# Kernel tuning notes

Measured on AMD Instinct MI355X. Metric: run time of the kernel, lower is better.

## Reference

```python
import jax, jax.numpy as jnp
import numpy as np

NUM_OPS = 100_000
NUM_MACH = 512
H = 128
OPF = 6
MF = 2
L = 2
N_PREC = 800_000
N_CHALF = 800_000  # compat edges per direction
EPS = 1e-5


def setup_inputs() -> dict:
    key = jax.random.key(0)
    ks = jax.random.split(key, 20)
    op_features = jax.random.normal(ks[0], (NUM_OPS, OPF), dtype=jnp.float32)
    machine_features = jax.random.normal(ks[1], (NUM_MACH, MF), dtype=jnp.float32)
    prec_src = jax.random.randint(ks[2], (N_PREC,), 0, NUM_OPS, dtype=jnp.int32)
    prec_tgt = jax.random.randint(ks[3], (N_PREC,), 0, NUM_OPS, dtype=jnp.int32)
    precedence_edges = jnp.stack([prec_src, prec_tgt])  # [2, N_PREC]
    op_idx = jax.random.randint(ks[4], (N_CHALF,), 0, NUM_OPS, dtype=jnp.int32)
    m_idx = jax.random.randint(ks[5], (N_CHALF,), 0, NUM_MACH, dtype=jnp.int32)
    # bidirectional pairs in unified node space (machines offset by NUM_OPS)
    src = jnp.concatenate([op_idx, m_idx + NUM_OPS])
    tgt = jnp.concatenate([m_idx + NUM_OPS, op_idx])
    compatibility_edges = jnp.stack([src, tgt])  # [2, 2*N_CHALF]
    s = 0.05
    op_emb_W = jax.random.normal(ks[6], (H, OPF), dtype=jnp.float32) * s
    op_emb_b = jnp.zeros((H,), jnp.float32)
    mach_emb_W = jax.random.normal(ks[7], (H, MF), dtype=jnp.float32) * s
    mach_emb_b = jnp.zeros((H,), jnp.float32)
    prec_W = jax.random.normal(ks[8], (L, H, H), dtype=jnp.float32) * s
    prec_b = jax.random.normal(ks[9], (L, H), dtype=jnp.float32) * s
    compat_W = jax.random.normal(ks[10], (L, H, H), dtype=jnp.float32) * s
    compat_b = jax.random.normal(ks[11], (L, H), dtype=jnp.float32) * s
    op_ln_g = jnp.ones((L, H), jnp.float32)
    op_ln_b = jnp.zeros((L, H), jnp.float32)
    mach_ln_g = jnp.ones((L, H), jnp.float32)
    mach_ln_b = jnp.zeros((L, H), jnp.float32)
    return dict(op_features=op_features, machine_features=machine_features,
                precedence_edges=precedence_edges, compatibility_edges=compatibility_edges,
                op_emb_W=op_emb_W, op_emb_b=op_emb_b, mach_emb_W=mach_emb_W, mach_emb_b=mach_emb_b,
                prec_W=prec_W, prec_b=prec_b, compat_W=compat_W, compat_b=compat_b,
                op_ln_g=op_ln_g, op_ln_b=op_ln_b, mach_ln_g=mach_ln_g, mach_ln_b=mach_ln_b)


def _layer_norm(x, g, b):
    mu = jnp.mean(x, axis=-1, keepdims=True)
    var = jnp.mean(jnp.square(x - mu), axis=-1, keepdims=True)
    return (x - mu) * jax.lax.rsqrt(var + EPS) * g + b


def _scatter_mean(vals, idx, mask, n):
    # vals [E,H], idx [E], mask [E] bool (or None); mean over incoming edges, count clamped >= 1
    if mask is not None:
        vals = jnp.where(mask[:, None], vals, 0.0)
        idx = jnp.where(mask, idx, 0)
        ones = mask.astype(vals.dtype)
    else:
        ones = jnp.ones(idx.shape, vals.dtype)
    sums = jax.ops.segment_sum(vals, idx, num_segments=n)
    cnts = jax.ops.segment_sum(ones, idx, num_segments=n)
    return sums / jnp.maximum(cnts, 1.0)[:, None]


def _forward(op_features, machine_features, precedence_edges, compatibility_edges,
             op_emb_W, op_emb_b, mach_emb_W, mach_emb_b,
             prec_W, prec_b, compat_W, compat_b,
             op_ln_g, op_ln_b, mach_ln_g, mach_ln_b):
    num_ops = op_features.shape[0]
    num_mach = machine_features.shape[0]
    op_emb = op_features @ op_emb_W.T + op_emb_b
    mach_emb = machine_features @ mach_emb_W.T + mach_emb_b

    p_src, p_tgt = precedence_edges[0], precedence_edges[1]
    c_src, c_tgt = compatibility_edges[0], compatibility_edges[1]
    op2m = (c_src < num_ops) & (c_tgt >= num_ops)
    m2o = (c_src >= num_ops) & (c_tgt < num_ops)
    o2m_src = jnp.where(op2m, c_src, 0)
    o2m_tgt = jnp.where(op2m, c_tgt - num_ops, 0)
    m2o_src = jnp.where(m2o, c_src - num_ops, 0)
    m2o_tgt = jnp.where(m2o, c_tgt, 0)

    for l in range(L):
        # precedence (op -> op): linear-then-gather == gather-then-linear
        op_t = op_emb @ prec_W[l].T + prec_b[l]            # [num_ops, H]
        op_emb_prec = _scatter_mean(op_t[p_src], p_tgt, None, num_ops)
        # compatibility, shared linear for both directions
        op_c = op_emb @ compat_W[l].T + compat_b[l]        # [num_ops, H]
        mach_c = mach_emb @ compat_W[l].T + compat_b[l]    # [num_mach, H]
        mach_emb_compat = _scatter_mean(op_c[o2m_src], o2m_tgt, op2m, num_mach)
        op_emb_compat = _scatter_mean(mach_c[m2o_src], m2o_tgt, m2o, num_ops)
        op_emb = _layer_norm(op_emb + op_emb_prec + op_emb_compat, op_ln_g[l], op_ln_b[l])
        mach_emb = _layer_norm(mach_emb + mach_emb_compat, mach_ln_g[l], mach_ln_b[l])
    return op_emb, mach_emb


def reference(op_features, machine_features, precedence_edges, compatibility_edges,
              op_emb_W, op_emb_b, mach_emb_W, mach_emb_b,
              prec_W, prec_b, compat_W, compat_b,
              op_ln_g, op_ln_b, mach_ln_g, mach_ln_b):
    return _forward(op_features, machine_features, precedence_edges, compatibility_edges,
                    op_emb_W, op_emb_b, mach_emb_W, mach_emb_b,
                    prec_W, prec_b, compat_W, compat_b,
                    op_ln_g, op_ln_b, mach_ln_g, mach_ln_b)
```

## Files before the change

kernel.cpp:

```cpp
#include <hip/hip_runtime.h>
#include <hip/hip_bf16.h>

#define NUM_OPS   100000
#define NUM_MACH  512
#define HDIM      128
#define P1        100352
#define NHIST     200704
#define NBLK      196
#define NCOARSE   784
#define NBC       256
#define NBM       256
#define MHWORDS   (NUM_MACH * NBM)
#define NBLK_M    128

typedef short short8 __attribute__((ext_vector_type(8)));
typedef float floatx4 __attribute__((ext_vector_type(4)));

__device__ __forceinline__ unsigned short f2bf(float f) {
    unsigned u = __float_as_uint(f);
    unsigned r = (u + 0x7FFFu + ((u >> 16) & 1u)) >> 16;
    return (unsigned short)r;
}
__device__ __forceinline__ float bf2f(unsigned short u) {
    return __uint_as_float(((unsigned)u) << 16);
}

__global__ void k_embed(const float* __restrict__ F,
                        const float* __restrict__ W,
                        const float* __restrict__ b,
                        float* __restrict__ out,
                        unsigned short* __restrict__ outb, int M, int FD) {
    int idx = blockIdx.x * blockDim.x + threadIdx.x;
    if (idx >= M * HDIM) return;
    int r = idx >> 7, h = idx & 127;
    const float* f = F + (size_t)r * FD;
    const float* w = W + (size_t)h * FD;
    float s = b[h];
    for (int i = 0; i < FD; ++i) s += f[i] * w[i];
    out[idx] = s;
    if (outb) outb[idx] = f2bf(s);
}

__global__ void k_wconv(const float* __restrict__ Wp, const float* __restrict__ Wc,
                        unsigned short* __restrict__ Wb) {
    int i = blockIdx.x * blockDim.x + threadIdx.x;
    if (i >= 2 * 128 * 256) return;
    int l = i >> 15, h = (i >> 8) & 127, k = i & 255;
    float v = (k < 128) ? Wp[(size_t)l * 16384 + h * 128 + k]
                        : Wc[(size_t)l * 16384 + h * 128 + (k - 128)];
    Wb[i] = f2bf(v);
}

__global__ __launch_bounds__(256) void k_chist(const int* __restrict__ prec_e, int nprec,
                                               const int* __restrict__ comp_e, int E,
                                               int* __restrict__ blockhist) {
    __shared__ int h[NCOARSE];
    for (int i = threadIdx.x; i < NCOARSE; i += 256) h[i] = 0;
    __syncthreads();
    int NT = nprec + E;
    int ch = (NT + NBC - 1) / NBC;
    int i0 = blockIdx.x * ch, i1 = min(NT, i0 + ch);
    for (int i = i0 + threadIdx.x; i < i1; i += 256) {
        int key = (i < nprec) ? prec_e[nprec + i] : (P1 + comp_e[i - nprec]);
        atomicAdd(&h[key >> 8], 1);
    }
    __syncthreads();
    for (int i = threadIdx.x; i < NCOARSE; i += 256)
        blockhist[i * NBC + blockIdx.x] = h[i];
}

__global__ __launch_bounds__(256) void k_cfill(const int* __restrict__ prec_e, int nprec,
                                               const int* __restrict__ comp_e, int E, int M,
                                               const int* __restrict__ scan,
                                               int* __restrict__ pairs) {
    __shared__ int cur[NCOARSE];
    for (int i = threadIdx.x; i < NCOARSE; i += 256) cur[i] = scan[i * NBC + blockIdx.x];
    __syncthreads();
    int NT = nprec + E;
    int ch = (NT + NBC - 1) / NBC;
    int i0 = blockIdx.x * ch, i1 = min(NT, i0 + ch);
    for (int i = i0 + threadIdx.x; i < i1; i += 256) {
        int key, val;
        if (i < nprec) { key = prec_e[nprec + i]; val = prec_e[i]; }
        else { int e = i - nprec; key = P1 + comp_e[e]; val = comp_e[E + e] - M; }
        int pos = atomicAdd(&cur[key >> 8], 1);
        pairs[pos] = (val << 8) | (key & 255);
    }
}

__global__ __launch_bounds__(256) void k_fine(const int* __restrict__ scan,
                                              const int* __restrict__ pairs, int NT,
                                              int* __restrict__ rs,
                                              int* __restrict__ bucket_all) {
    __shared__ int hh[256];
    __shared__ int ex[256];
    __shared__ int cu[256];
    int b = blockIdx.x, t = threadIdx.x;
    int s = scan[b * NBC];
    int e = (b == NCOARSE - 1) ? NT : scan[(b + 1) * NBC];
    hh[t] = 0;
    __syncthreads();
    for (int i = s + t; i < e; i += 256) atomicAdd(&hh[pairs[i] & 255], 1);
    __syncthreads();
    int v = hh[t];
    ex[t] = v; __syncthreads();
    for (int o = 1; o < 256; o <<= 1) {
        int x = (t >= o) ? ex[t - o] : 0; __syncthreads();
        ex[t] += x; __syncthreads();
    }
    int start = s + ex[t] - v;
    rs[b * 256 + t] = start;
    cu[t] = start;
    __syncthreads();
    for (int i = s + t; i < e; i += 256) {
        int p = pairs[i];
        int pos = atomicAdd(&cu[p & 255], 1);
        bucket_all[pos] = ((unsigned)p) >> 8;
    }
}

__global__ __launch_bounds__(256) void k_mhist(const int* __restrict__ comp_e, int E, int M,
                                               int* __restrict__ blockhist) {
    __shared__ int h[NUM_MACH];
    for (int i = threadIdx.x; i < NUM_MACH; i += 256) h[i] = 0;
    __syncthreads();
    int blk = blockIdx.x;
    int ch = (E + NBM - 1) / NBM;
    int e0 = blk * ch, e1 = min(E, e0 + ch);
    for (int e = e0 + threadIdx.x; e < e1; e += 256)
        atomicAdd(&h[comp_e[E + e] - M], 1);
    __syncthreads();
    for (int i = threadIdx.x; i < NUM_MACH; i += 256)
        blockhist[i * NBM + blk] = h[i];
}

__global__ __launch_bounds__(256) void k_blocksum(const int* __restrict__ arr, int* __restrict__ partial) {
    __shared__ int sh[256];
    int b = blockIdx.x, t = threadIdx.x;
    int4 v = *(const int4*)(arr + b * 1024 + t * 4);
    sh[t] = v.x + v.y + v.z + v.w;
    __syncthreads();
    for (int o = 128; o; o >>= 1) { if (t < o) sh[t] += sh[t + o]; __syncthreads(); }
    if (!t) partial[b] = sh[0];
}

__global__ __launch_bounds__(256) void k_scanpart(const int* __restrict__ partial, int n,
                                                  int* __restrict__ block_off) {
    __shared__ int sh[256];
    int t = threadIdx.x;
    int v = (t < n) ? partial[t] : 0;
    sh[t] = v; __syncthreads();
    for (int o = 1; o < 256; o <<= 1) {
        int x = (t >= o) ? sh[t - o] : 0; __syncthreads();
        sh[t] += x; __syncthreads();
    }
    if (t < n) block_off[t] = sh[t] - v;
}

__global__ __launch_bounds__(256) void k_scanwrite(const int* __restrict__ arr,
                                                   const int* __restrict__ block_off,
                                                   int* __restrict__ rs, int* __restrict__ cur) {
    __shared__ int sh[256];
    int b = blockIdx.x, t = threadIdx.x;
    int base_i = b * 1024 + t * 4;
    int4 v = *(const int4*)(arr + base_i);
    int tsum = v.x + v.y + v.z + v.w;
    sh[t] = tsum; __syncthreads();
    for (int o = 1; o < 256; o <<= 1) {
        int x = (t >= o) ? sh[t - o] : 0; __syncthreads();
        sh[t] += x; __syncthreads();
    }
    int off = block_off[b] + sh[t] - tsum;
    int4 r; r.x = off; r.y = off + v.x; r.z = off + v.x + v.y; r.w = off + v.x + v.y + v.z;
    *(int4*)(rs + base_i) = r;
    if (cur) *(int4*)(cur + base_i) = r;
}

__global__ void k_machrs(const int* __restrict__ moff, int* __restrict__ mach_rs, int E) {
    int t = threadIdx.x;
    for (int m = t; m < NUM_MACH; m += 256) mach_rs[m] = moff[m * NBM];
    if (t == 0) mach_rs[NUM_MACH] = E;
}

__global__ __launch_bounds__(256) void k_fill_mach(const int* __restrict__ comp_e, int E, int M,
                                                   const int* __restrict__ moff,
                                                   int* __restrict__ bucket_mach) {
    __shared__ int cur[NUM_MACH];
    int blk = blockIdx.x;
    for (int i = threadIdx.x; i < NUM_MACH; i += 256) cur[i] = moff[i * NBM + blk];
    __syncthreads();
    int ch = (E + NBM - 1) / NBM;
    int e0 = blk * ch, e1 = min(E, e0 + ch);
    for (int e = e0 + threadIdx.x; e < e1; e += 256) {
        int m = comp_e[E + e] - M;
        int op = comp_e[e];
        int pos = atomicAdd(&cur[m], 1);
        bucket_mach[pos] = op;
    }
}

__global__ __launch_bounds__(256) void k_agg_op(
    const unsigned short* __restrict__ op_ebf, const float* __restrict__ mach_emb,
    const int* __restrict__ rs, const int* __restrict__ bucket_all,
    unsigned short* __restrict__ Ab, int* __restrict__ flags, int M) {
    int wave = threadIdx.x >> 6, lane = threadIdx.x & 63;
    int r = blockIdx.x * 4 + wave;
    if (r >= M) return;
    int h = lane * 2;

    float a0 = 0.f, a1 = 0.f;
    int s0 = rs[r], e0 = rs[r + 1];
    for (int base = s0; base < e0; base += 64) {
        int cnt = min(64, e0 - base);
        int idx = (lane < cnt) ? bucket_all[base + lane] : 0;
        for (int j = 0; j < cnt; j += 4) {
            int i0 = __shfl(idx, j);
            int i1 = __shfl(idx, j + 1);
            int i2 = __shfl(idx, j + 2);
            int i3 = __shfl(idx, j + 3);
            ushort2 v0 = *(const ushort2*)(op_ebf + (size_t)i0 * HDIM + h);
            ushort2 v1 = *(const ushort2*)(op_ebf + (size_t)i1 * HDIM + h);
            ushort2 v2 = *(const ushort2*)(op_ebf + (size_t)i2 * HDIM + h);
            ushort2 v3 = *(const ushort2*)(op_ebf + (size_t)i3 * HDIM + h);
            a0 += bf2f(v0.x); a1 += bf2f(v0.y);
            if (j + 1 < cnt) { a0 += bf2f(v1.x); a1 += bf2f(v1.y); }
            if (j + 2 < cnt) { a0 += bf2f(v2.x); a1 += bf2f(v2.y); }
            if (j + 3 < cnt) { a0 += bf2f(v3.x); a1 += bf2f(v3.y); }
        }
    }
    float pinv = 1.f / fmaxf((float)(e0 - s0), 1.f);

    float b0 = 0.f, b1 = 0.f;
    int s1 = rs[P1 + r], e1 = rs[P1 + r + 1];
    for (int base = s1; base < e1; base += 64) {
        int cnt = min(64, e1 - base);
        int idx = (lane < cnt) ? bucket_all[base + lane] : 0;
        for (int j = 0; j < cnt; j += 4) {
            int i0 = __shfl(idx, j);
            int i1 = __shfl(idx, j + 1);
            int i2 = __shfl(idx, j + 2);
            int i3 = __shfl(idx, j + 3);
            float2 v0 = *(const float2*)(mach_emb + (size_t)i0 * HDIM + h);
            float2 v1 = *(const float2*)(mach_emb + (size_t)i1 * HDIM + h);
            float2 v2 = *(const float2*)(mach_emb + (size_t)i2 * HDIM + h);
            float2 v3 = *(const float2*)(mach_emb + (size_t)i3 * HDIM + h);
            b0 += v0.x; b1 += v0.y;
            if (j + 1 < cnt) { b0 += v1.x; b1 += v1.y; }
            if (j + 2 < cnt) { b0 += v2.x; b1 += v2.y; }
            if (j + 3 < cnt) { b0 += v3.x; b1 += v3.y; }
        }
    }
    float cinv = 1.f / fmaxf((float)(e1 - s1), 1.f);

    ushort2 pa, pb;
    pa.x = f2bf(a0 * pinv); pa.y = f2bf(a1 * pinv);
    pb.x = f2bf(b0 * cinv); pb.y = f2bf(b1 * cinv);
    *(ushort2*)(Ab + (size_t)r * 256 + h)       = pa;
    *(ushort2*)(Ab + (size_t)r * 256 + 128 + h) = pb;
    if (lane == 0) flags[r] = (e0 > s0 ? 1 : 0) | (e1 > s1 ? 2 : 0);
}

__global__ __launch_bounds__(256) void k_gemm_mfma(
    const unsigned short* __restrict__ Ab, const float* __restrict__ emb,
    const unsigned short* __restrict__ Wb,
    const float* __restrict__ bp, const float* __restrict__ bc,
    const int* __restrict__ flags,
    const float* __restrict__ g, const float* __restrict__ bt,
    float* __restrict__ dst, unsigned short* __restrict__ dstb, int M) {
    int wave = threadIdx.x >> 6, lane = threadIdx.x & 63;
    int m0 = blockIdx.x * 64 + wave * 16;
    if (m0 >= M) return;
    int quad = lane >> 4, col = lane & 15;

    floatx4 acc[8];
#pragma unroll
    for (int t = 0; t < 8; ++t) acc[t] = (floatx4){0.f, 0.f, 0.f, 0.f};

    const short* Arow  = (const short*)(Ab + (size_t)(m0 + col) * 256);
    const short* Wbase = (const short*)Wb;

#pragma unroll
    for (int ks = 0; ks < 8; ++ks) {
        short8 a = *(const short8*)(Arow + ks * 32 + quad * 8);
#pragma unroll
        for (int t = 0; t < 8; ++t) {
            short8 b = *(const short8*)(Wbase + (size_t)(t * 16 + col) * 256 + ks * 32 + quad * 8);
            acc[t] = __builtin_amdgcn_mfma_f32_16x16x32_bf16(a, b, acc[t], 0, 0, 0);
        }
    }

    float bpv[8], bcv[8], gv[8], btv[8];
#pragma unroll
    for (int t = 0; t < 8; ++t) {
        int c = t * 16 + col;
        bpv[t] = bp[c]; bcv[t] = bc[c]; gv[t] = g[c]; btv[t] = bt[c];
    }
#pragma unroll
    for (int reg = 0; reg < 4; ++reg) {
        int r = m0 + quad * 4 + reg;
        int fl = flags[r];
        float fp = (fl & 1) ? 1.f : 0.f, fc = (fl & 2) ? 1.f : 0.f;
        float x[8]; float s = 0.f, q = 0.f;
#pragma unroll
        for (int t = 0; t < 8; ++t) {
            float v = acc[t][reg] + emb[(size_t)r * HDIM + t * 16 + col] + fp * bpv[t] + fc * bcv[t];
            x[t] = v; s += v; q += v * v;
        }
#pragma unroll
        for (int msk = 1; msk < 16; msk <<= 1) { s += __shfl_xor(s, msk); q += __shfl_xor(q, msk); }
        float mu = s * (1.f / 128.f);
        float rstd = rsqrtf(fmaxf(q * (1.f / 128.f) - mu * mu, 0.f) + 1e-5f);
#pragma unroll
        for (int t = 0; t < 8; ++t) {
            float y = (x[t] - mu) * rstd * gv[t] + btv[t];
            dst[(size_t)r * HDIM + t * 16 + col] = y;
            if (dstb) dstb[(size_t)r * HDIM + t * 16 + col] = f2bf(y);
        }
    }
}

__global__ __launch_bounds__(256) void k_mach_gather(
    const int* __restrict__ mach_rs, const int* __restrict__ bucket_mach,
    const unsigned short* __restrict__ op_ebf, float* __restrict__ mach_sum) {
    int m = blockIdx.x;
    int t = threadIdx.x;
    int wave = t >> 6, lane = t & 63;
    int h = lane * 2;
    int s0 = mach_rs[m], e0 = mach_rs[m + 1];
    float a0 = 0.f, a1 = 0.f;
    for (int base = s0 + (blockIdx.y * 4 + wave) * 64; base < e0; base += gridDim.y * 256) {
        int cnt = min(64, e0 - base);
        int idx = (lane < cnt) ? bucket_mach[base + lane] : 0;
        for (int j = 0; j < cnt; j += 4) {
            int i0 = __shfl(idx, j);
            int i1 = __shfl(idx, j + 1);
            int i2 = __shfl(idx, j + 2);
            int i3 = __shfl(idx, j + 3);
            ushort2 v0 = *(const ushort2*)(op_ebf + (size_t)i0 * HDIM + h);
            ushort2 v1 = *(const ushort2*)(op_ebf + (size_t)i1 * HDIM + h);
            ushort2 v2 = *(const ushort2*)(op_ebf + (size_t)i2 * HDIM + h);
            ushort2 v3 = *(const ushort2*)(op_ebf + (size_t)i3 * HDIM + h);
            a0 += bf2f(v0.x); a1 += bf2f(v0.y);
            if (j + 1 < cnt) { a0 += bf2f(v1.x); a1 += bf2f(v1.y); }
            if (j + 2 < cnt) { a0 += bf2f(v2.x); a1 += bf2f(v2.y); }
            if (j + 3 < cnt) { a0 += bf2f(v3.x); a1 += bf2f(v3.y); }
        }
    }
    atomicAdd(&mach_sum[m * HDIM + h], a0);
    atomicAdd(&mach_sum[m * HDIM + h + 1], a1);
}

__global__ __launch_bounds__(128) void k_mach_update(
    const float* __restrict__ mach_emb, const float* __restrict__ mach_sum,
    const int* __restrict__ mach_rs,
    const float* __restrict__ Wc, const float* __restrict__ bc,
    const float* __restrict__ g, const float* __restrict__ bt,
    float* __restrict__ dst) {
    __shared__ float row[HDIM];
    __shared__ float red[4];
    int m = blockIdx.x, t = threadIdx.x;
    int cnt = mach_rs[m + 1] - mach_rs[m];
    float sc = (cnt > 0) ? 1.f / (float)cnt : 0.f;
    row[t] = mach_sum[m * HDIM + t] * sc;
    __syncthreads();
    float dot = bc[t];
    const float* w = Wc + (size_t)t * HDIM;
#pragma unroll 8
    for (int k = 0; k < HDIM; ++k) dot += row[k] * w[k];
    float x = mach_emb[m * HDIM + t] + ((cnt > 0) ? dot : 0.f);
    float s = x, q = x * x;
#pragma unroll
    for (int o = 32; o; o >>= 1) { s += __shfl_xor(s, o); q += __shfl_xor(q, o); }
    int wv = t >> 6;
    if ((t & 63) == 0) { red[wv * 2] = s; red[wv * 2 + 1] = q; }
    __syncthreads();
    s = red[0] + red[2]; q = red[1] + red[3];
    float mu = s * (1.f / 128.f);
    float rstd = rsqrtf(fmaxf(q * (1.f / 128.f) - mu * mu, 0.f) + 1e-5f);
    dst[m * HDIM + t] = (x - mu) * rstd * g[t] + bt[t];
}

extern "C" void kernel_launch(void* const* d_in, const int* in_sizes, int n_in,
                              void* d_out, int out_size, void* d_ws, size_t ws_size,
                              hipStream_t stream) {
    const float* op_feat    = (const float*)d_in[0];
    const float* m_feat     = (const float*)d_in[1];
    const int*   prec_e     = (const int*)d_in[2];
    const int*   comp_e     = (const int*)d_in[3];
    const float* op_emb_W   = (const float*)d_in[4];
    const float* op_emb_b   = (const float*)d_in[5];
    const float* mach_emb_W = (const float*)d_in[6];
    const float* mach_emb_b = (const float*)d_in[7];
    const float* prec_W     = (const float*)d_in[8];
    const float* prec_b     = (const float*)d_in[9];
    const float* compat_W   = (const float*)d_in[10];
    const float* compat_b   = (const float*)d_in[11];
    const float* op_ln_g    = (const float*)d_in[12];
    const float* op_ln_b    = (const float*)d_in[13];
    const float* mach_ln_g  = (const float*)d_in[14];
    const float* mach_ln_b  = (const float*)d_in[15];
    float* out = (float*)d_out;

    const int M = NUM_OPS, NM = NUM_MACH;
    const int nprec = in_sizes[2] / 2;
    const int ncomp = in_sizes[3] / 2;
    const int E = ncomp / 2;
    const int NT = nprec + E;

    float* ws = (float*)d_ws;
    size_t o = 0;
    float* op_emb   = ws + o; o += (size_t)M * HDIM;
    unsigned short* op_ebf = (unsigned short*)(ws + o); o += (size_t)M * 64;
    unsigned short* Ab = (unsigned short*)(ws + o); o += (size_t)M * 128;
    unsigned short* Wb = (unsigned short*)(ws + o); o += 32768;
    float* mach_emb = ws + o; o += (size_t)NM * HDIM;
    float* mach_sum = ws + o; o += (size_t)NM * HDIM;
    int* ip = (int*)(ws + o);
    size_t io = 0;
    int* chist     = ip + io; io += NHIST;
    int* rs        = ip + io; io += NHIST;
    int* cscan     = ip + io; io += NHIST;
    int* blockhist = ip + io; io += MHWORDS;
    int* moff      = ip + io; io += MHWORDS;
    int* mach_rs   = ip + io; io += NM + 8;
    int* partialA  = ip + io; io += 256;
    int* block_offA= ip + io; io += 256;
    int* partialB  = ip + io; io += 256;
    int* block_offB= ip + io; io += 256;
    int* flags     = ip + io; io += M;
    int* pairs     = ip + io; io += (size_t)NT;
    int* bucket_all  = ip + io; io += (size_t)NT;
    int* bucket_mach = ip + io; io += (size_t)E;

    k_chist<<<NBC, 256, 0, stream>>>(prec_e, nprec, comp_e, E, chist);
    k_mhist<<<NBM, 256, 0, stream>>>(comp_e, E, M, blockhist);
    k_blocksum<<<NBLK, 256, 0, stream>>>(chist, partialA);
    k_scanpart<<<1, 256, 0, stream>>>(partialA, NBLK, block_offA);
    k_scanwrite<<<NBLK, 256, 0, stream>>>(chist, block_offA, cscan, nullptr);
    k_blocksum<<<NBLK_M, 256, 0, stream>>>(blockhist, partialB);
    k_scanpart<<<1, 256, 0, stream>>>(partialB, NBLK_M, block_offB);
    k_scanwrite<<<NBLK_M, 256, 0, stream>>>(blockhist, block_offB, moff, nullptr);
    k_machrs<<<1, 256, 0, stream>>>(moff, mach_rs, E);
    k_cfill<<<NBC, 256, 0, stream>>>(prec_e, nprec, comp_e, E, M, cscan, pairs);
    k_fine<<<NCOARSE, 256, 0, stream>>>(cscan, pairs, NT, rs, bucket_all);
    k_fill_mach<<<NBM, 256, 0, stream>>>(comp_e, E, M, moff, bucket_mach);

    k_embed<<<(M * HDIM + 255) / 256, 256, 0, stream>>>(op_feat, op_emb_W, op_emb_b, op_emb, op_ebf, M, 6);
    k_embed<<<(NM * HDIM + 255) / 256, 256, 0, stream>>>(m_feat, mach_emb_W, mach_emb_b, mach_emb, nullptr, NM, 2);
    k_wconv<<<(2 * 128 * 256 + 255) / 256, 256, 0, stream>>>(prec_W, compat_W, Wb);

    for (int l = 0; l < 2; ++l) {
        int last = (l == 1);
        const float* bpl = prec_b   + (size_t)l * HDIM;
        const float* Wc  = compat_W + (size_t)l * HDIM * HDIM;
        const float* bcl = compat_b + (size_t)l * HDIM;

        hipMemsetAsync(mach_sum, 0, (size_t)NM * HDIM * sizeof(float), stream);

        k_agg_op<<<(M + 3) / 4, 256, 0, stream>>>(op_ebf, mach_emb, rs, bucket_all, Ab, flags, M);
        k_mach_gather<<<dim3(NM, 4), 256, 0, stream>>>(mach_rs, bucket_mach, op_ebf, mach_sum);

        k_gemm_mfma<<<(M + 63) / 64, 256, 0, stream>>>(
            Ab, op_emb, Wb + (size_t)l * 128 * 256, bpl, bcl, flags,
            op_ln_g + (size_t)l * HDIM, op_ln_b + (size_t)l * HDIM,
            last ? out : op_emb, last ? nullptr : op_ebf, M);

        k_mach_update<<<NM, 128, 0, stream>>>(
            mach_emb, mach_sum, mach_rs, Wc, bcl,
            mach_ln_g + (size_t)l * HDIM, mach_ln_b + (size_t)l * HDIM,
            last ? (out + (size_t)M * HDIM) : mach_emb);
    }
}
```

Before: 583.2 us.

## Fuse op aggregation into MFMA GEMM kernel via swizzled LDS tile

The per-op neighbour aggregation (precedence and compatibility means) moves into the GEMM+LayerNorm kernel. Each wave gathers its 16 rows into a swizzled 64x256 bf16 shared-memory tile, and edge-presence flags are packed into a register. This removes the global Ab intermediate and flags buffer round trip and one launch per layer. The bf16 op embedding is now ping-ponged between two buffers, because the fused kernel writes new embeddings while other rows still read the old ones, and the machine gather is reordered to run afterwards. The cost is that each wave gathers its 16 rows one after another, and the 32KB of LDS per block lowers occupancy, which may reduce memory-level parallelism for the random gathers.

Result: slower. 732.6 us (+25.6%).

```diff
diff --git a/kernel.cpp b/kernel.cpp
--- a/kernel.cpp
+++ b/kernel.cpp
@@ -199,89 +199,90 @@
     }
 }
 
-__global__ __launch_bounds__(256) void k_agg_op(
+__global__ __launch_bounds__(256) void k_fused(
     const unsigned short* __restrict__ op_ebf, const float* __restrict__ mach_emb,
     const int* __restrict__ rs, const int* __restrict__ bucket_all,
-    unsigned short* __restrict__ Ab, int* __restrict__ flags, int M) {
-    int wave = threadIdx.x >> 6, lane = threadIdx.x & 63;
-    int r = blockIdx.x * 4 + wave;
-    if (r >= M) return;
-    int h = lane * 2;
-
-    float a0 = 0.f, a1 = 0.f;
-    int s0 = rs[r], e0 = rs[r + 1];
-    for (int base = s0; base < e0; base += 64) {
-        int cnt = min(64, e0 - base);
-        int idx = (lane < cnt) ? bucket_all[base + lane] : 0;
-        for (int j = 0; j < cnt; j += 4) {
-            int i0 = __shfl(idx, j);
-            int i1 = __shfl(idx, j + 1);
-            int i2 = __shfl(idx, j + 2);
-            int i3 = __shfl(idx, j + 3);
-            ushort2 v0 = *(const ushort2*)(op_ebf + (size_t)i0 * HDIM + h);
-            ushort2 v1 = *(const ushort2*)(op_ebf + (size_t)i1 * HDIM + h);
-            ushort2 v2 = *(const ushort2*)(op_ebf + (size_t)i2 * HDIM + h);
-            ushort2 v3 = *(const ushort2*)(op_ebf + (size_t)i3 * HDIM + h);
-            a0 += bf2f(v0.x); a1 += bf2f(v0.y);
-            if (j + 1 < cnt) { a0 += bf2f(v1.x); a1 += bf2f(v1.y); }
-            if (j + 2 < cnt) { a0 += bf2f(v2.x); a1 += bf2f(v2.y); }
-            if (j + 3 < cnt) { a0 += bf2f(v3.x); a1 += bf2f(v3.y); }
-        }
-    }
-    float pinv = 1.f / fmaxf((float)(e0 - s0), 1.f);
-
-    float b0 = 0.f, b1 = 0.f;
-    int s1 = rs[P1 + r], e1 = rs[P1 + r + 1];
-    for (int base = s1; base < e1; base += 64) {
-        int cnt = min(64, e1 - base);
-        int idx = (lane < cnt) ? bucket_all[base + lane] : 0;
-        for (int j = 0; j < cnt; j += 4) {
-            int i0 = __shfl(idx, j);
-            int i1 = __shfl(idx, j + 1);
-            int i2 = __shfl(idx, j + 2);
-            int i3 = __shfl(idx, j + 3);
-            float2 v0 = *(const float2*)(mach_emb + (size_t)i0 * HDIM + h);
-            float2 v1 = *(const float2*)(mach_emb + (size_t)i1 * HDIM + h);
-            float2 v2 = *(const float2*)(mach_emb + (size_t)i2 * HDIM + h);
-            float2 v3 = *(const float2*)(mach_emb + (size_t)i3 * HDIM + h);
-            b0 += v0.x; b1 += v0.y;
-            if (j + 1 < cnt) { b0 += v1.x; b1 += v1.y; }
-            if (j + 2 < cnt) { b0 += v2.x; b1 += v2.y; }
-            if (j + 3 < cnt) { b0 += v3.x; b1 += v3.y; }
-        }
-    }
-    float cinv = 1.f / fmaxf((float)(e1 - s1), 1.f);
-
-    ushort2 pa, pb;
-    pa.x = f2bf(a0 * pinv); pa.y = f2bf(a1 * pinv);
-    pb.x = f2bf(b0 * cinv); pb.y = f2bf(b1 * cinv);
-    *(ushort2*)(Ab + (size_t)r * 256 + h)       = pa;
-    *(ushort2*)(Ab + (size_t)r * 256 + 128 + h) = pb;
-    if (lane == 0) flags[r] = (e0 > s0 ? 1 : 0) | (e1 > s1 ? 2 : 0);
-}
-
-__global__ __launch_bounds__(256) void k_gemm_mfma(
-    const unsigned short* __restrict__ Ab, const float* __restrict__ emb,
+    const float* __restrict__ emb,
     const unsigned short* __restrict__ Wb,
     const float* __restrict__ bp, const float* __restrict__ bc,
-    const int* __restrict__ flags,
     const float* __restrict__ g, const float* __restrict__ bt,
     float* __restrict__ dst, unsigned short* __restrict__ dstb, int M) {
+    __shared__ unsigned short At[64 * 256];
     int wave = threadIdx.x >> 6, lane = threadIdx.x & 63;
     int m0 = blockIdx.x * 64 + wave * 16;
     if (m0 >= M) return;
+    int h = lane * 2;
+    unsigned fl_packed = 0;
+
+    for (int i = 0; i < 16; ++i) {
+        int r = m0 + i;
+        int ri = wave * 16 + i;
+
+        float a0 = 0.f, a1 = 0.f;
+        int s0 = rs[r], e0 = rs[r + 1];
+        for (int base = s0; base < e0; base += 64) {
+            int cnt = min(64, e0 - base);
+            int idx = (lane < cnt) ? bucket_all[base + lane] : 0;
+            for (int j = 0; j < cnt; j += 4) {
+                int i0 = __shfl(idx, j);
+                int i1 = __shfl(idx, j + 1);
+                int i2 = __shfl(idx, j + 2);
+                int i3 = __shfl(idx, j + 3);
+                ushort2 v0 = *(const ushort2*)(op_ebf + (size_t)i0 * HDIM + h);
+                ushort2 v1 = *(const ushort2*)(op_ebf + (size_t)i1 * HDIM + h);
+                ushort2 v2 = *(const ushort2*)(op_ebf + (size_t)i2 * HDIM + h);
+                ushort2 v3 = *(const ushort2*)(op_ebf + (size_t)i3 * HDIM + h);
+                a0 += bf2f(v0.x); a1 += bf2f(v0.y);
+                if (j + 1 < cnt) { a0 += bf2f(v1.x); a1 += bf2f(v1.y); }
+                if (j + 2 < cnt) { a0 += bf2f(v2.x); a1 += bf2f(v2.y); }
+                if (j + 3 < cnt) { a0 += bf2f(v3.x); a1 += bf2f(v3.y); }
+            }
+        }
+        float pinv = 1.f / fmaxf((float)(e0 - s0), 1.f);
+
+        float b0 = 0.f, b1 = 0.f;
+        int s1 = rs[P1 + r], e1 = rs[P1 + r + 1];
+        for (int base = s1; base < e1; base += 64) {
+            int cnt = min(64, e1 - base);
+            int idx = (lane < cnt) ? bucket_all[base + lane] : 0;
+            for (int j = 0; j < cnt; j += 4) {
+                int i0 = __shfl(idx, j);
+                int i1 = __shfl(idx, j + 1);
+                int i2 = __shfl(idx, j + 2);
+                int i3 = __shfl(idx, j + 3);
+                float2 v0 = *(const float2*)(mach_emb + (size_t)i0 * HDIM + h);
+                float2 v1 = *(const float2*)(mach_emb + (size_t)i1 * HDIM + h);
+                float2 v2 = *(const float2*)(mach_emb + (size_t)i2 * HDIM + h);
+                float2 v3 = *(const float2*)(mach_emb + (size_t)i3 * HDIM + h);
+                b0 += v0.x; b1 += v0.y;
+                if (j + 1 < cnt) { b0 += v1.x; b1 += v1.y; }
+                if (j + 2 < cnt) { b0 += v2.x; b1 += v2.y; }
+                if (j + 3 < cnt) { b0 += v3.x; b1 += v3.y; }
+            }
+        }
+        float cinv = 1.f / fmaxf((float)(e1 - s1), 1.f);
+
+        ushort2 pa, pb;
+        pa.x = f2bf(a0 * pinv); pa.y = f2bf(a1 * pinv);
+        pb.x = f2bf(b0 * cinv); pb.y = f2bf(b1 * cinv);
+        unsigned sw = (ri & 7) << 4;
+        *(ushort2*)((char*)At + ri * 512 + ((lane * 4) ^ sw))       = pa;
+        *(ushort2*)((char*)At + ri * 512 + ((256 + lane * 4) ^ sw)) = pb;
+        fl_packed |= ((e0 > s0 ? 1u : 0u) | (e1 > s1 ? 2u : 0u)) << (2 * i);
+    }
+
     int quad = lane >> 4, col = lane & 15;
+    int ri = wave * 16 + col;
+    unsigned swr = (ri & 7) << 4;
 
     floatx4 acc[8];
 #pragma unroll
     for (int t = 0; t < 8; ++t) acc[t] = (floatx4){0.f, 0.f, 0.f, 0.f};
 
-    const short* Arow  = (const short*)(Ab + (size_t)(m0 + col) * 256);
     const short* Wbase = (const short*)Wb;
-
 #pragma unroll
     for (int ks = 0; ks < 8; ++ks) {
-        short8 a = *(const short8*)(Arow + ks * 32 + quad * 8);
+        short8 a = *(const short8*)((const char*)At + ri * 512 + ((ks * 64 + quad * 16) ^ swr));
 #pragma unroll
         for (int t = 0; t < 8; ++t) {
             short8 b = *(const short8*)(Wbase + (size_t)(t * 16 + col) * 256 + ks * 32 + quad * 8);
@@ -298,7 +299,7 @@
 #pragma unroll
     for (int reg = 0; reg < 4; ++reg) {
         int r = m0 + quad * 4 + reg;
-        int fl = flags[r];
+        int fl = (fl_packed >> ((quad * 4 + reg) * 2)) & 3;
         float fp = (fl & 1) ? 1.f : 0.f, fc = (fl & 2) ? 1.f : 0.f;
         float x[8]; float s = 0.f, q = 0.f;
 #pragma unroll
@@ -410,8 +411,8 @@
     float* ws = (float*)d_ws;
     size_t o = 0;
     float* op_emb   = ws + o; o += (size_t)M * HDIM;
-    unsigned short* op_ebf = (unsigned short*)(ws + o); o += (size_t)M * 64;
-    unsigned short* Ab = (unsigned short*)(ws + o); o += (size_t)M * 128;
+    unsigned short* op_ebfA = (unsigned short*)(ws + o); o += (size_t)M * 64;
+    unsigned short* op_ebfB = (unsigned short*)(ws + o); o += (size_t)M * 64;
     unsigned short* Wb = (unsigned short*)(ws + o); o += 32768;
     float* mach_emb = ws + o; o += (size_t)NM * HDIM;
     float* mach_sum = ws + o; o += (size_t)NM * HDIM;
@@ -427,7 +428,6 @@
     int* block_offA= ip + io; io += 256;
     int* partialB  = ip + io; io += 256;
     int* block_offB= ip + io; io += 256;
-    int* flags     = ip + io; io += M;
     int* pairs     = ip + io; io += (size_t)NT;
     int* bucket_all  = ip + io; io += (size_t)NT;
     int* bucket_mach = ip + io; io += (size_t)E;
@@ -445,25 +445,27 @@
     k_fine<<<NCOARSE, 256, 0, stream>>>(cscan, pairs, NT, rs, bucket_all);
     k_fill_mach<<<NBM, 256, 0, stream>>>(comp_e, E, M, moff, bucket_mach);
 
-    k_embed<<<(M * HDIM + 255) / 256, 256, 0, stream>>>(op_feat, op_emb_W, op_emb_b, op_emb, op_ebf, M, 6);
+    k_embed<<<(M * HDIM + 255) / 256, 256, 0, stream>>>(op_feat, op_emb_W, op_emb_b, op_emb, op_ebfA, M, 6);
     k_embed<<<(NM * HDIM + 255) / 256, 256, 0, stream>>>(m_feat, mach_emb_W, mach_emb_b, mach_emb, nullptr, NM, 2);
     k_wconv<<<(2 * 128 * 256 + 255) / 256, 256, 0, stream>>>(prec_W, compat_W, Wb);
 
     for (int l = 0; l < 2; ++l) {
         int last = (l == 1);
+        const unsigned short* ebf_src = (l == 0) ? op_ebfA : op_ebfB;
+        unsigned short* ebf_dst = (l == 0) ? op_ebfB : nullptr;
         const float* bpl = prec_b   + (size_t)l * HDIM;
         const float* Wc  = compat_W + (size_t)l * HDIM * HDIM;
         const float* bcl = compat_b + (size_t)l * HDIM;
 
         hipMemsetAsync(mach_sum, 0, (size_t)NM * HDIM * sizeof(float), stream);
 
-        k_agg_op<<<(M + 3) / 4, 256, 0, stream>>>(op_ebf, mach_emb, rs, bucket_all, Ab, flags, M);
-        k_mach_gather<<<dim3(NM, 4), 256, 0, stream>>>(mach_rs, bucket_mach, op_ebf, mach_sum);
-
-        k_gemm_mfma<<<(M + 63) / 64, 256, 0, stream>>>(
-            Ab, op_emb, Wb + (size_t)l * 128 * 256, bpl, bcl, flags,
+        k_fused<<<(M + 63) / 64, 256, 0, stream>>>(
+            ebf_src, mach_emb, rs, bucket_all, op_emb,
+            Wb + (size_t)l * 128 * 256, bpl, bcl,
             op_ln_g + (size_t)l * HDIM, op_ln_b + (size_t)l * HDIM,
-            last ? out : op_emb, last ? nullptr : op_ebf, M);
+            last ? out : op_emb, ebf_dst, M);
+
+        k_mach_gather<<<dim3(NM, 4), 256, 0, stream>>>(mach_rs, bucket_mach, ebf_src, mach_sum);
 
         k_mach_update<<<NM, 128, 0, stream>>>(
             mach_emb, mach_sum, mach_rs, Wc, bcl,
```

## Merge preprocessing and aggregation kernels to cut launch count

Applied to the files above, without the earlier changes.

Several small kernels are fused into fewer launches. The coarse and machine histograms are built in one pass, and both scans are batched into single blocksum/scanpart/scanwrite launches. The fine bucket fill is merged with the machine fill, the three embedding and weight-conversion kernels become one, and op aggregation is merged with the machine gather, which now uses 16-byte short8 loads. The aim is to remove launch overhead and serialization between small kernels, at the cost of branchy mixed-role grids and a machine partition tied to the NT chunking.

Result: no change. 579.1 us (-0.7%).

```diff
diff --git a/kernel.cpp b/kernel.cpp
--- a/kernel.cpp
+++ b/kernel.cpp
@@ -12,6 +12,7 @@
 #define NBM       256
 #define MHWORDS   (NUM_MACH * NBM)
 #define NBLK_M    128
+#define NBLK_T    (NBLK + NBLK_M)
 
 typedef short short8 __attribute__((ext_vector_type(8)));
 typedef float floatx4 __attribute__((ext_vector_type(4)));
@@ -25,48 +26,68 @@
     return __uint_as_float(((unsigned)u) << 16);
 }
 
-__global__ void k_embed(const float* __restrict__ F,
-                        const float* __restrict__ W,
-                        const float* __restrict__ b,
-                        float* __restrict__ out,
-                        unsigned short* __restrict__ outb, int M, int FD) {
+__global__ void k_prep(const float* __restrict__ Fo, const float* __restrict__ Fm,
+                       const float* __restrict__ Wo, const float* __restrict__ bo,
+                       const float* __restrict__ Wm, const float* __restrict__ bm,
+                       const float* __restrict__ Wp, const float* __restrict__ Wc,
+                       float* __restrict__ op_emb, unsigned short* __restrict__ op_ebf,
+                       float* __restrict__ mach_emb, unsigned short* __restrict__ Wb) {
     int idx = blockIdx.x * blockDim.x + threadIdx.x;
-    if (idx >= M * HDIM) return;
-    int r = idx >> 7, h = idx & 127;
-    const float* f = F + (size_t)r * FD;
-    const float* w = W + (size_t)h * FD;
-    float s = b[h];
-    for (int i = 0; i < FD; ++i) s += f[i] * w[i];
-    out[idx] = s;
-    if (outb) outb[idx] = f2bf(s);
-}
-
-__global__ void k_wconv(const float* __restrict__ Wp, const float* __restrict__ Wc,
-                        unsigned short* __restrict__ Wb) {
-    int i = blockIdx.x * blockDim.x + threadIdx.x;
-    if (i >= 2 * 128 * 256) return;
-    int l = i >> 15, h = (i >> 8) & 127, k = i & 255;
-    float v = (k < 128) ? Wp[(size_t)l * 16384 + h * 128 + k]
-                        : Wc[(size_t)l * 16384 + h * 128 + (k - 128)];
-    Wb[i] = f2bf(v);
-}
-
-__global__ __launch_bounds__(256) void k_chist(const int* __restrict__ prec_e, int nprec,
-                                               const int* __restrict__ comp_e, int E,
-                                               int* __restrict__ blockhist) {
-    __shared__ int h[NCOARSE];
-    for (int i = threadIdx.x; i < NCOARSE; i += 256) h[i] = 0;
+    if (idx < NUM_OPS * HDIM) {
+        int r = idx >> 7, h = idx & 127;
+        const float* f = Fo + (size_t)r * 6;
+        const float* w = Wo + (size_t)h * 6;
+        float s = bo[h];
+#pragma unroll
+        for (int i = 0; i < 6; ++i) s += f[i] * w[i];
+        op_emb[idx] = s;
+        op_ebf[idx] = f2bf(s);
+        return;
+    }
+    idx -= NUM_OPS * HDIM;
+    if (idx < NUM_MACH * HDIM) {
+        int r = idx >> 7, h = idx & 127;
+        const float* f = Fm + (size_t)r * 2;
+        const float* w = Wm + (size_t)h * 2;
+        mach_emb[idx] = bm[h] + f[0] * w[0] + f[1] * w[1];
+        return;
+    }
+    idx -= NUM_MACH * HDIM;
+    if (idx < 2 * 128 * 256) {
+        int l = idx >> 15, h = (idx >> 8) & 127, k = idx & 255;
+        float v = (k < 128) ? Wp[(size_t)l * 16384 + h * 128 + k]
+                            : Wc[(size_t)l * 16384 + h * 128 + (k - 128)];
+        Wb[idx] = f2bf(v);
+    }
+}
+
+__global__ __launch_bounds__(256) void k_front(const int* __restrict__ prec_e, int nprec,
+                                               const int* __restrict__ comp_e, int E, int M,
+                                               int* __restrict__ chist_bh,
+                                               int* __restrict__ mach_bh) {
+    __shared__ int hc[NCOARSE];
+    __shared__ int hm[NUM_MACH];
+    for (int i = threadIdx.x; i < NCOARSE; i += 256) hc[i] = 0;
+    for (int i = threadIdx.x; i < NUM_MACH; i += 256) hm[i] = 0;
     __syncthreads();
     int NT = nprec + E;
     int ch = (NT + NBC - 1) / NBC;
     int i0 = blockIdx.x * ch, i1 = min(NT, i0 + ch);
     for (int i = i0 + threadIdx.x; i < i1; i += 256) {
-        int key = (i < nprec) ? prec_e[nprec + i] : (P1 + comp_e[i - nprec]);
-        atomicAdd(&h[key >> 8], 1);
+        int key;
+        if (i < nprec) key = prec_e[nprec + i];
+        else {
+            int e = i - nprec;
+            key = P1 + comp_e[e];
+            atomicAdd(&hm[comp_e[E + e] - M], 1);
+        }
+        atomicAdd(&hc[key >> 8], 1);
     }
     __syncthreads();
     for (int i = threadIdx.x; i < NCOARSE; i += 256)
-        blockhist[i * NBC + blockIdx.x] = h[i];
+        chist_bh[i * NBC + blockIdx.x] = hc[i];
+    for (int i = threadIdx.x; i < NUM_MACH; i += 256)
+        mach_bh[i * NBC + blockIdx.x] = hm[i];
 }
 
 __global__ __launch_bounds__(256) void k_cfill(const int* __restrict__ prec_e, int nprec,
@@ -88,52 +109,6 @@
     }
 }
 
-__global__ __launch_bounds__(256) void k_fine(const int* __restrict__ scan,
-                                              const int* __restrict__ pairs, int NT,
-                                              int* __restrict__ rs,
-                                              int* __restrict__ bucket_all) {
-    __shared__ int hh[256];
-    __shared__ int ex[256];
-    __shared__ int cu[256];
-    int b = blockIdx.x, t = threadIdx.x;
-    int s = scan[b * NBC];
-    int e = (b == NCOARSE - 1) ? NT : scan[(b + 1) * NBC];
-    hh[t] = 0;
-    __syncthreads();
-    for (int i = s + t; i < e; i += 256) atomicAdd(&hh[pairs[i] & 255], 1);
-    __syncthreads();
-    int v = hh[t];
-    ex[t] = v; __syncthreads();
-    for (int o = 1; o < 256; o <<= 1) {
-        int x = (t >= o) ? ex[t - o] : 0; __syncthreads();
-        ex[t] += x; __syncthreads();
-    }
-    int start = s + ex[t] - v;
-    rs[b * 256 + t] = start;
-    cu[t] = start;
-    __syncthreads();
-    for (int i = s + t; i < e; i += 256) {
-        int p = pairs[i];
-        int pos = atomicAdd(&cu[p & 255], 1);
-        bucket_all[pos] = ((unsigned)p) >> 8;
-    }
-}
-
-__global__ __launch_bounds__(256) void k_mhist(const int* __restrict__ comp_e, int E, int M,
-                                               int* __restrict__ blockhist) {
-    __shared__ int h[NUM_MACH];
-    for (int i = threadIdx.x; i < NUM_MACH; i += 256) h[i] = 0;
-    __syncthreads();
-    int blk = blockIdx.x;
-    int ch = (E + NBM - 1) / NBM;
-    int e0 = blk * ch, e1 = min(E, e0 + ch);
-    for (int e = e0 + threadIdx.x; e < e1; e += 256)
-        atomicAdd(&h[comp_e[E + e] - M], 1);
-    __syncthreads();
-    for (int i = threadIdx.x; i < NUM_MACH; i += 256)
-        blockhist[i * NBM + blk] = h[i];
-}
-
 __global__ __launch_bounds__(256) void k_blocksum(const int* __restrict__ arr, int* __restrict__ partial) {
     __shared__ int sh[256];
     int b = blockIdx.x, t = threadIdx.x;
@@ -144,22 +119,24 @@
     if (!t) partial[b] = sh[0];
 }
 
-__global__ __launch_bounds__(256) void k_scanpart(const int* __restrict__ partial, int n,
+__global__ __launch_bounds__(256) void k_scanpart(const int* __restrict__ partial,
                                                   int* __restrict__ block_off) {
     __shared__ int sh[256];
     int t = threadIdx.x;
-    int v = (t < n) ? partial[t] : 0;
+    int seg0 = blockIdx.x ? NBLK : 0;
+    int n    = blockIdx.x ? NBLK_M : NBLK;
+    int v = (t < n) ? partial[seg0 + t] : 0;
     sh[t] = v; __syncthreads();
     for (int o = 1; o < 256; o <<= 1) {
         int x = (t >= o) ? sh[t - o] : 0; __syncthreads();
         sh[t] += x; __syncthreads();
     }
-    if (t < n) block_off[t] = sh[t] - v;
+    if (t < n) block_off[seg0 + t] = sh[t] - v;
 }
 
 __global__ __launch_bounds__(256) void k_scanwrite(const int* __restrict__ arr,
                                                    const int* __restrict__ block_off,
-                                                   int* __restrict__ rs, int* __restrict__ cur) {
+                                                   int* __restrict__ rs) {
     __shared__ int sh[256];
     int b = blockIdx.x, t = threadIdx.x;
     int base_i = b * 1024 + t * 4;
@@ -173,91 +150,164 @@
     int off = block_off[b] + sh[t] - tsum;
     int4 r; r.x = off; r.y = off + v.x; r.z = off + v.x + v.y; r.w = off + v.x + v.y + v.z;
     *(int4*)(rs + base_i) = r;
-    if (cur) *(int4*)(cur + base_i) = r;
-}
-
-__global__ void k_machrs(const int* __restrict__ moff, int* __restrict__ mach_rs, int E) {
+}
+
+__global__ __launch_bounds__(256) void k_finefill(const int* __restrict__ scans, int NT,
+                                                  const int* __restrict__ pairs,
+                                                  int* __restrict__ rs,
+                                                  int* __restrict__ bucket_all,
+                                                  const int* __restrict__ comp_e, int E, int M,
+                                                  int* __restrict__ bucket_mach,
+                                                  int* __restrict__ mach_rs) {
     int t = threadIdx.x;
-    for (int m = t; m < NUM_MACH; m += 256) mach_rs[m] = moff[m * NBM];
-    if (t == 0) mach_rs[NUM_MACH] = E;
-}
-
-__global__ __launch_bounds__(256) void k_fill_mach(const int* __restrict__ comp_e, int E, int M,
-                                                   const int* __restrict__ moff,
-                                                   int* __restrict__ bucket_mach) {
-    __shared__ int cur[NUM_MACH];
-    int blk = blockIdx.x;
-    for (int i = threadIdx.x; i < NUM_MACH; i += 256) cur[i] = moff[i * NBM + blk];
-    __syncthreads();
-    int ch = (E + NBM - 1) / NBM;
-    int e0 = blk * ch, e1 = min(E, e0 + ch);
-    for (int e = e0 + threadIdx.x; e < e1; e += 256) {
-        int m = comp_e[E + e] - M;
-        int op = comp_e[e];
-        int pos = atomicAdd(&cur[m], 1);
-        bucket_mach[pos] = op;
-    }
-}
-
-__global__ __launch_bounds__(256) void k_agg_op(
+    if (blockIdx.x < NCOARSE) {
+        __shared__ int hh[256];
+        __shared__ int ex[256];
+        __shared__ int cu[256];
+        int b = blockIdx.x;
+        int s = scans[b * NBC];
+        int e = (b == NCOARSE - 1) ? NT : scans[(b + 1) * NBC];
+        hh[t] = 0;
+        __syncthreads();
+        for (int i = s + t; i < e; i += 256) atomicAdd(&hh[pairs[i] & 255], 1);
+        __syncthreads();
+        int v = hh[t];
+        ex[t] = v; __syncthreads();
+        for (int o = 1; o < 256; o <<= 1) {
+            int x = (t >= o) ? ex[t - o] : 0; __syncthreads();
+            ex[t] += x; __syncthreads();
+        }
+        int start = s + ex[t] - v;
+        rs[b * 256 + t] = start;
+        cu[t] = start;
+        __syncthreads();
+        for (int i = s + t; i < e; i += 256) {
+            int p = pairs[i];
+            int pos = atomicAdd(&cu[p & 255], 1);
+            bucket_all[pos] = ((unsigned)p) >> 8;
+        }
+    } else {
+        __shared__ int cur[NUM_MACH];
+        int blk = blockIdx.x - NCOARSE;
+        const int* moff = scans + NHIST;
+        for (int i = t; i < NUM_MACH; i += 256) cur[i] = moff[i * NBM + blk];
+        if (blk == 0) {
+            for (int m = t; m < NUM_MACH; m += 256) mach_rs[m] = moff[m * NBM];
+            if (t == 0) mach_rs[NUM_MACH] = E;
+        }
+        __syncthreads();
+        int nprec = NT - E;
+        int chNT = (NT + NBC - 1) / NBC;
+        int e0 = blk * chNT - nprec;       if (e0 < 0) e0 = 0;
+        int e1 = (blk + 1) * chNT - nprec; if (e1 > E) e1 = E;
+        for (int e = e0 + t; e < e1; e += 256) {
+            int m = comp_e[E + e] - M;
+            int op = comp_e[e];
+            int pos = atomicAdd(&cur[m], 1);
+            bucket_mach[pos] = op;
+        }
+    }
+}
+
+__global__ __launch_bounds__(256) void k_aggmg(
     const unsigned short* __restrict__ op_ebf, const float* __restrict__ mach_emb,
     const int* __restrict__ rs, const int* __restrict__ bucket_all,
-    unsigned short* __restrict__ Ab, int* __restrict__ flags, int M) {
+    unsigned short* __restrict__ Ab, int* __restrict__ flags, int M,
+    const int* __restrict__ mach_rs, const int* __restrict__ bucket_mach,
+    float* __restrict__ mach_sum, int nb_agg) {
     int wave = threadIdx.x >> 6, lane = threadIdx.x & 63;
-    int r = blockIdx.x * 4 + wave;
-    if (r >= M) return;
-    int h = lane * 2;
-
-    float a0 = 0.f, a1 = 0.f;
-    int s0 = rs[r], e0 = rs[r + 1];
-    for (int base = s0; base < e0; base += 64) {
+
+    if ((int)blockIdx.x < nb_agg) {
+        int r = blockIdx.x * 4 + wave;
+        if (r >= M) return;
+        int h = lane * 2;
+
+        float a0 = 0.f, a1 = 0.f;
+        int s0 = rs[r], e0 = rs[r + 1];
+        for (int base = s0; base < e0; base += 64) {
+            int cnt = min(64, e0 - base);
+            int idx = (lane < cnt) ? bucket_all[base + lane] : 0;
+            for (int j = 0; j < cnt; j += 4) {
+                int i0 = __shfl(idx, j);
+                int i1 = __shfl(idx, j + 1);
+                int i2 = __shfl(idx, j + 2);
+                int i3 = __shfl(idx, j + 3);
+                ushort2 v0 = *(const ushort2*)(op_ebf + (size_t)i0 * HDIM + h);
+                ushort2 v1 = *(const ushort2*)(op_ebf + (size_t)i1 * HDIM + h);
+                ushort2 v2 = *(const ushort2*)(op_ebf + (size_t)i2 * HDIM + h);
+                ushort2 v3 = *(const ushort2*)(op_ebf + (size_t)i3 * HDIM + h);
+                a0 += bf2f(v0.x); a1 += bf2f(v0.y);
+                if (j + 1 < cnt) { a0 += bf2f(v1.x); a1 += bf2f(v1.y); }
+                if (j + 2 < cnt) { a0 += bf2f(v2.x); a1 += bf2f(v2.y); }
+                if (j + 3 < cnt) { a0 += bf2f(v3.x); a1 += bf2f(v3.y); }
+            }
+        }
+        float pinv = 1.f / fmaxf((float)(e0 - s0), 1.f);
+
+        float b0 = 0.f, b1 = 0.f;
+        int s1 = rs[P1 + r], e1 = rs[P1 + r + 1];
+        for (int base = s1; base < e1; base += 64) {
+            int cnt = min(64, e1 - base);
+            int idx = (lane < cnt) ? bucket_all[base + lane] : 0;
+            for (int j = 0; j < cnt; j += 4) {
+                int i0 = __shfl(idx, j);
+                int i1 = __shfl(idx, j + 1);
+                int i2 = __shfl(idx, j + 2);
+                int i3 = __shfl(idx, j + 3);
+                float2 v0 = *(const float2*)(mach_emb + (size_t)i0 * HDIM + h);
+                float2 v1 = *(const float2*)(mach_emb + (size_t)i1 * HDIM + h);
+                float2 v2 = *(const float2*)(mach_emb + (size_t)i2 * HDIM + h);
+                float2 v3 = *(const float2*)(mach_emb + (size_t)i3 * HDIM + h);
+                b0 += v0.x; b1 += v0.y;
+                if (j + 1 < cnt) { b0 += v1.x; b1 += v1.y; }
+                if (j + 2 < cnt) { b0 += v2.x; b1 += v2.y; }
+                if (j + 3 < cnt) { b0 += v3.x; b1 += v3.y; }
+            }
+        }
+        float cinv = 1.f / fmaxf((float)(e1 - s1), 1.f);
+
+        ushort2 pa, pb;
+        pa.x = f2bf(a0 * pinv); pa.y = f2bf(a1 * pinv);
+        pb.x = f2bf(b0 * cinv); pb.y = f2bf(b1 * cinv);
+        *(ushort2*)(Ab + (size_t)r * 256 + h)       = pa;
+        *(ushort2*)(Ab + (size_t)r * 256 + 128 + h) = pb;
+        if (lane == 0) flags[r] = (e0 > s0 ? 1 : 0) | (e1 > s1 ? 2 : 0);
+        return;
+    }
+
+    int b2 = blockIdx.x - nb_agg;
+    int m  = b2 & 511;
+    int yq = b2 >> 9;
+    int g  = lane >> 4;
+    int d  = (lane & 15) * 8;
+    int s0 = mach_rs[m], e0 = mach_rs[m + 1];
+    float a[8];
+#pragma unroll
+    for (int k = 0; k < 8; ++k) a[k] = 0.f;
+
+    for (int base = s0 + (yq * 4 + wave) * 64; base < e0; base += 1024) {
         int cnt = min(64, e0 - base);
-        int idx = (lane < cnt) ? bucket_all[base + lane] : 0;
+        int idx = (lane < cnt) ? bucket_mach[base + lane] : 0;
         for (int j = 0; j < cnt; j += 4) {
-            int i0 = __shfl(idx, j);
-            int i1 = __shfl(idx, j + 1);
-            int i2 = __shfl(idx, j + 2);
-            int i3 = __shfl(idx, j + 3);
-            ushort2 v0 = *(const ushort2*)(op_ebf + (size_t)i0 * HDIM + h);
-            ushort2 v1 = *(const ushort2*)(op_ebf + (size_t)i1 * HDIM + h);
-            ushort2 v2 = *(const ushort2*)(op_ebf + (size_t)i2 * HDIM + h);
-            ushort2 v3 = *(const ushort2*)(op_ebf + (size_t)i3 * HDIM + h);
-            a0 += bf2f(v0.x); a1 += bf2f(v0.y);
-            if (j + 1 < cnt) { a0 += bf2f(v1.x); a1 += bf2f(v1.y); }
-            if (j + 2 < cnt) { a0 += bf2f(v2.x); a1 += bf2f(v2.y); }
-            if (j + 3 < cnt) { a0 += bf2f(v3.x); a1 += bf2f(v3.y); }
-        }
-    }
-    float pinv = 1.f / fmaxf((float)(e0 - s0), 1.f);
-
-    float b0 = 0.f, b1 = 0.f;
-    int s1 = rs[P1 + r], e1 = rs[P1 + r + 1];
-    for (int base = s1; base < e1; base += 64) {
-        int cnt = min(64, e1 - base);
-        int idx = (lane < cnt) ? bucket_all[base + lane] : 0;
-        for (int j = 0; j < cnt; j += 4) {
-            int i0 = __shfl(idx, j);
-            int i1 = __shfl(idx, j + 1);
-            int i2 = __shfl(idx, j + 2);
-            int i3 = __shfl(idx, j + 3);
-            float2 v0 = *(const float2*)(mach_emb + (size_t)i0 * HDIM + h);
-            float2 v1 = *(const float2*)(mach_emb + (size_t)i1 * HDIM + h);
-            float2 v2 = *(const float2*)(mach_emb + (size_t)i2 * HDIM + h);
-            float2 v3 = *(const float2*)(mach_emb + (size_t)i3 * HDIM + h);
-            b0 += v0.x; b1 += v0.y;
-            if (j + 1 < cnt) { b0 += v1.x; b1 += v1.y; }
-            if (j + 2 < cnt) { b0 += v2.x; b1 += v2.y; }
-            if (j + 3 < cnt) { b0 += v3.x; b1 += v3.y; }
-        }
-    }
-    float cinv = 1.f / fmaxf((float)(e1 - s1), 1.f);
-
-    ushort2 pa, pb;
-    pa.x = f2bf(a0 * pinv); pa.y = f2bf(a1 * pinv);
-    pb.x = f2bf(b0 * cinv); pb.y = f2bf(b1 * cinv);
-    *(ushort2*)(Ab + (size_t)r * 256 + h)       = pa;
-    *(ushort2*)(Ab + (size_t)r * 256 + 128 + h) = pb;
-    if (lane == 0) flags[r] = (e0 > s0 ? 1 : 0) | (e1 > s1 ? 2 : 0);
+            int jj = j + g;
+            int rowi = __shfl(idx, jj);
+            short8 v = *(const short8*)(op_ebf + (size_t)rowi * HDIM + d);
+            if (jj < cnt) {
+#pragma unroll
+                for (int k = 0; k < 8; ++k) a[k] += bf2f((unsigned short)v[k]);
+            }
+        }
+    }
+#pragma unroll
+    for (int k = 0; k < 8; ++k) {
+        a[k] += __shfl_xor(a[k], 16);
+        a[k] += __shfl_xor(a[k], 32);
+    }
+    if (lane < 16) {
+#pragma unroll
+        for (int k = 0; k < 8; ++k)
+            atomicAdd(&mach_sum[m * HDIM + d + k], a[k]);
+    }
 }
 
 __global__ __launch_bounds__(256) void k_gemm_mfma(
@@ -317,37 +367,6 @@
             if (dstb) dstb[(size_t)r * HDIM + t * 16 + col] = f2bf(y);
         }
     }
-}
-
-__global__ __launch_bounds__(256) void k_mach_gather(
-    const int* __restrict__ mach_rs, const int* __restrict__ bucket_mach,
-    const unsigned short* __restrict__ op_ebf, float* __restrict__ mach_sum) {
-    int m = blockIdx.x;
-    int t = threadIdx.x;
-    int wave = t >> 6, lane = t & 63;
-    int h = lane * 2;
-    int s0 = mach_rs[m], e0 = mach_rs[m + 1];
-    float a0 = 0.f, a1 = 0.f;
-    for (int base = s0 + (blockIdx.y * 4 + wave) * 64; base < e0; base += gridDim.y * 256) {
-        int cnt = min(64, e0 - base);
-        int idx = (lane < cnt) ? bucket_mach[base + lane] : 0;
-        for (int j = 0; j < cnt; j += 4) {
-            int i0 = __shfl(idx, j);
-            int i1 = __shfl(idx, j + 1);
-            int i2 = __shfl(idx, j + 2);
-            int i3 = __shfl(idx, j + 3);
-            ushort2 v0 = *(const ushort2*)(op_ebf + (size_t)i0 * HDIM + h);
-            ushort2 v1 = *(const ushort2*)(op_ebf + (size_t)i1 * HDIM + h);
-            ushort2 v2 = *(const ushort2*)(op_ebf + (size_t)i2 * HDIM + h);
-            ushort2 v3 = *(const ushort2*)(op_ebf + (size_t)i3 * HDIM + h);
-            a0 += bf2f(v0.x); a1 += bf2f(v0.y);
-            if (j + 1 < cnt) { a0 += bf2f(v1.x); a1 += bf2f(v1.y); }
-            if (j + 2 < cnt) { a0 += bf2f(v2.x); a1 += bf2f(v2.y); }
-            if (j + 3 < cnt) { a0 += bf2f(v3.x); a1 += bf2f(v3.y); }
-        }
-    }
-    atomicAdd(&mach_sum[m * HDIM + h], a0);
-    atomicAdd(&mach_sum[m * HDIM + h + 1], a1);
 }
 
 __global__ __launch_bounds__(128) void k_mach_update(
@@ -417,38 +436,33 @@
     float* mach_sum = ws + o; o += (size_t)NM * HDIM;
     int* ip = (int*)(ws + o);
     size_t io = 0;
-    int* chist     = ip + io; io += NHIST;
+    int* hists     = ip + io; io += NHIST + MHWORDS;
+    int* scans     = ip + io; io += NHIST + MHWORDS;
     int* rs        = ip + io; io += NHIST;
-    int* cscan     = ip + io; io += NHIST;
-    int* blockhist = ip + io; io += MHWORDS;
-    int* moff      = ip + io; io += MHWORDS;
     int* mach_rs   = ip + io; io += NM + 8;
-    int* partialA  = ip + io; io += 256;
-    int* block_offA= ip + io; io += 256;
-    int* partialB  = ip + io; io += 256;
-    int* block_offB= ip + io; io += 256;
+    int* partialT  = ip + io; io += 512;
+    int* block_off = ip + io; io += 512;
     int* flags     = ip + io; io += M;
     int* pairs     = ip + io; io += (size_t)NT;
     int* bucket_all  = ip + io; io += (size_t)NT;
     int* bucket_mach = ip + io; io += (size_t)E;
 
-    k_chist<<<NBC, 256, 0, stream>>>(prec_e, nprec, comp_e, E, chist);
-    k_mhist<<<NBM, 256, 0, stream>>>(comp_e, E, M, blockhist);
-    k_blocksum<<<NBLK, 256, 0, stream>>>(chist, partialA);
-    k_scanpart<<<1, 256, 0, stream>>>(partialA, NBLK, block_offA);
-    k_scanwrite<<<NBLK, 256, 0, stream>>>(chist, block_offA, cscan, nullptr);
-    k_blocksum<<<NBLK_M, 256, 0, stream>>>(blockhist, partialB);
-    k_scanpart<<<1, 256, 0, stream>>>(partialB, NBLK_M, block_offB);
-    k_scanwrite<<<NBLK_M, 256, 0, stream>>>(blockhist, block_offB, moff, nullptr);
-    k_machrs<<<1, 256, 0, stream>>>(moff, mach_rs, E);
-    k_cfill<<<NBC, 256, 0, stream>>>(prec_e, nprec, comp_e, E, M, cscan, pairs);
-    k_fine<<<NCOARSE, 256, 0, stream>>>(cscan, pairs, NT, rs, bucket_all);
-    k_fill_mach<<<NBM, 256, 0, stream>>>(comp_e, E, M, moff, bucket_mach);
-
-    k_embed<<<(M * HDIM + 255) / 256, 256, 0, stream>>>(op_feat, op_emb_W, op_emb_b, op_emb, op_ebf, M, 6);
-    k_embed<<<(NM * HDIM + 255) / 256, 256, 0, stream>>>(m_feat, mach_emb_W, mach_emb_b, mach_emb, nullptr, NM, 2);
-    k_wconv<<<(2 * 128 * 256 + 255) / 256, 256, 0, stream>>>(prec_W, compat_W, Wb);
-
+    int* mach_bh = hists + NHIST;
+
+    k_front<<<NBC, 256, 0, stream>>>(prec_e, nprec, comp_e, E, M, hists, mach_bh);
+    k_blocksum<<<NBLK_T, 256, 0, stream>>>(hists, partialT);
+    k_scanpart<<<2, 256, 0, stream>>>(partialT, block_off);
+    k_scanwrite<<<NBLK_T, 256, 0, stream>>>(hists, block_off, scans);
+    k_cfill<<<NBC, 256, 0, stream>>>(prec_e, nprec, comp_e, E, M, scans, pairs);
+    k_finefill<<<NCOARSE + NBM, 256, 0, stream>>>(scans, NT, pairs, rs, bucket_all,
+                                                  comp_e, E, M, bucket_mach, mach_rs);
+
+    int prep_total = (M + NM) * HDIM + 2 * 128 * 256;
+    k_prep<<<(prep_total + 255) / 256, 256, 0, stream>>>(
+        op_feat, m_feat, op_emb_W, op_emb_b, mach_emb_W, mach_emb_b,
+        prec_W, compat_W, op_emb, op_ebf, mach_emb, Wb);
+
+    const int nb_agg = (M + 3) / 4;
     for (int l = 0; l < 2; ++l) {
         int last = (l == 1);
         const float* bpl = prec_b   + (size_t)l * HDIM;
@@ -457,8 +471,9 @@
 
         hipMemsetAsync(mach_sum, 0, (size_t)NM * HDIM * sizeof(float), stream);
 
-        k_agg_op<<<(M + 3) / 4, 256, 0, stream>>>(op_ebf, mach_emb, rs, bucket_all, Ab, flags, M);
-        k_mach_gather<<<dim3(NM, 4), 256, 0, stream>>>(mach_rs, bucket_mach, op_ebf, mach_sum);
+        k_aggmg<<<nb_agg + NM * 4, 256, 0, stream>>>(
+            op_ebf, mach_emb, rs, bucket_all, Ab, flags, M,
+            mach_rs, bucket_mach, mach_sum, nb_agg);
 
         k_gemm_mfma<<<(M + 63) / 64, 256, 0, stream>>>(
             Ab, op_emb, Wb + (size_t)l * 128 * 256, bpl, bcl, flags,
```
